# Kernel tuning notes

Measured on AMD Instinct MI355X. Metric: run time of the kernel, lower is better.

## Reference

```python
import jax, jax.numpy as jnp
import numpy as np

B, T, E = 8, 16384, 512
SEG = 16            # segment_count
DIL = 2             # dilation
DK = 64             # d_k
DV = 64             # d_v
POS_SCALE = 1.0     # pos_emb_scaling
L = T // SEG        # per-segment attention length before dilation (1024)
NORM = 1.0 / np.sqrt(DK)


def setup_inputs() -> dict:
    key = jax.random.key(0)
    k0, k1, k2, k3, k4 = jax.random.split(key, 5)
    x_in = jax.random.normal(k0, (B, T, E), dtype=jnp.float32)
    # parameters are drawn randn(k, m)/sqrt(k) in the original build
    Wk = jax.random.normal(k1, (DK, E), dtype=jnp.float32) / np.sqrt(DK)
    Wq = jax.random.normal(k2, (DK, E), dtype=jnp.float32) / np.sqrt(DK)
    Wv = jax.random.normal(k3, (DV, E), dtype=jnp.float32) / np.sqrt(DK)
    positional_embeddings_KQ = jax.random.normal(k4, (L, L), dtype=jnp.float32)
    return {"x_in": x_in, "Wk": Wk, "Wq": Wq, "Wv": Wv,
            "positional_embeddings_KQ": positional_embeddings_KQ}


def reference(x_in, Wk, Wq, Wv, positional_embeddings_KQ):
    # x_view: (B, SEG, E, L), then dilate last (time-within-segment) axis
    xv = x_in.reshape(B, L, SEG, E).transpose(0, 2, 3, 1)[:, :, :, ::DIL]  # (B,SEG,E,Ld)
    Q = jnp.einsum('bsel,ke->bslk', xv, Wq)  # (B,SEG,Ld,DK)
    K = jnp.einsum('bsel,ke->bslk', xv, Wk)
    V = jnp.einsum('bsel,ke->bslk', xv, Wv)  # (B,SEG,Ld,DV)
    # KQ[b,s,k,m] = <K_k, Q_m>
    KQ = jnp.einsum('bskd,bsmd->bskm', K, Q)  # (B,SEG,Ld,Ld)
    # causal tril mask, dilated; mask-fill with -inf (multiply-then-fill == where)
    mask = jnp.tril(jnp.ones((L, L), dtype=bool))[::DIL, ::DIL]
    KQ = jnp.where(mask, KQ, -jnp.inf)
    # positional bias (added after masking, as in the original)
    p = (positional_embeddings_KQ * POS_SCALE)[:L, :L][::DIL, ::DIL]
    KQ = KQ + p
    # NOTE: faithful to original — softmax over dim 3 (the Q/m axis)
    smKQ = jax.nn.softmax(KQ * NORM, axis=3)
    # att[b,s,m,d] = sum_n smKQ[b,s,n,m] * V[b,s,n,d]
    att = jnp.einsum('bsnm,bsnd->bsmd', smKQ, V)  # (B,SEG,Ld,DV)
    Ld = att.shape[2]
    # 'same' padding: strided scatter into zero-initialized (B,T,DV)
    res = jnp.zeros((B, T, DV), dtype=x_in.dtype)
    res = res.at[:, ::DIL, :].set(att.reshape(B, SEG * Ld, DV))
    return res
```

## Files before the change

### kernel.cpp

```cpp
#include <hip/hip_runtime.h>
#include <stdint.h>

typedef __attribute__((ext_vector_type(4))) float f32x4;
typedef __attribute__((ext_vector_type(8))) short bf16x8;
typedef __attribute__((ext_vector_type(4))) unsigned int u32x4;

#define C_NORM_LOG2E 0.18033688011112043f

__device__ __forceinline__ uint32_t swz(uint32_t a) { return a ^ (((a >> 7) & 7u) << 4); }
__device__ __forceinline__ uint32_t swzP(uint32_t a) { return a ^ (((a >> 7) & 3u) << 4); }

__device__ __forceinline__ uint32_t cvt_pk_bf16(float a, float b) {
  uint32_t r;
  asm("v_cvt_pk_bf16_f32 %0, %1, %2" : "=v"(r) : "v"(a), "v"(b));
  return r;
}

__device__ __forceinline__ float2 unpk_bf16(uint32_t u) {
  float2 f;
  f.x = __uint_as_float(u << 16);
  f.y = __uint_as_float(u & 0xffff0000u);
  return f;
}

__device__ __forceinline__ ushort f2bf(float f) {
  uint32_t u = __float_as_uint(f);
  u += 0x7FFFu + ((u >> 16) & 1u);
  return (ushort)(u >> 16);
}

__device__ __forceinline__ void gl_lds16(const void* gp, void* lp) {
  __builtin_amdgcn_global_load_lds((const __attribute__((address_space(1))) void*)gp,
                                   (__attribute__((address_space(3))) void*)lp, 16, 0, 0);
}

__global__ void pack_kernel(const float* __restrict__ Wk, const float* __restrict__ Wq,
                            const float* __restrict__ Wv, const float* __restrict__ PE,
                            ushort* __restrict__ Wp, float* __restrict__ PEdT) {
  int bid = blockIdx.x;
  if (bid < 384) {
    int i = bid * 256 + threadIdx.x;
    int n = i >> 9, e = i & 511;
    float val = (n < 64) ? Wq[n * 512 + e]
              : (n < 128) ? Wk[(n - 64) * 512 + e]
                          : Wv[(n - 128) * 512 + e];
    Wp[i] = f2bf(val);
  } else {
    int i = (bid - 384) * 256 + threadIdx.x;
    int m = i >> 9, n = i & 511;
    PEdT[i] = PE[n * 2048 + m * 2] * C_NORM_LOG2E;
  }
}

__global__ __launch_bounds__(512, 4) void proj_kernel(
    const float* __restrict__ x, const ushort* __restrict__ Wp,
    ushort* __restrict__ Qw, ushort* __restrict__ Kw, ushort* __restrict__ Vw) {
  __shared__ float Xl[2][8192];
  const int tid = threadIdx.x;
  const int lane = tid & 63, w = tid >> 6, g = lane >> 4, l15 = lane & 15;
  const int wr = w >> 2, wc = w & 3;
  const int bid = blockIdx.x;
  const int xcd = bid & 7, idx = bid >> 3;
  const int part = idx & 3, h = idx >> 2;
  const int bs = h * 8 + xcd;
  const int m0 = part * 128;
  const int R0 = bs * 512 + m0;
  const int b = bs >> 4, s = bs & 15;
  const char* xb = (const char*)x + ((size_t)b * 8388608 + (size_t)s * 512) * 4;

  f32x4 acc[4][3];
#pragma unroll
  for (int i = 0; i < 4; ++i)
#pragma unroll
    for (int j = 0; j < 3; ++j) acc[i][j] = (f32x4){0.f, 0.f, 0.f, 0.f};

  auto stage = [&](int kt, int buf) {
#pragma unroll
    for (int j = 0; j < 4; ++j) {
      uint32_t sl = (uint32_t)(j * 8192 + tid * 16);
      uint32_t t = sl ^ (((sl >> 8) & 7u) << 4);
      uint32_t row = t >> 8, colb = t & 255u;
      const char* src = xb + (size_t)(m0 + row) * 65536 + (size_t)kt * 256 + colb;
      gl_lds16(src, (char*)&Xl[buf][0] + sl);
    }
  };

  stage(0, 0);
  __syncthreads();
#pragma unroll
  for (int kt = 0; kt < 8; ++kt) {
    const int buf = kt & 1;
    if (kt < 7) stage(kt + 1, buf ^ 1);
#pragma unroll
    for (int kd = 0; kd < 2; ++kd) {
      bf16x8 bb[3];
#pragma unroll
      for (int j = 0; j < 3; ++j)
        bb[j] = *(const bf16x8*)((const char*)Wp + (size_t)(wc * 48 + j * 16 + l15) * 1024 +
                                 kt * 128 + kd * 64 + g * 16);
      bf16x8 a[4];
#pragma unroll
      for (int i = 0; i < 4; ++i) {
        int Rr = wr * 64 + i * 16 + l15;
        uint32_t a32 = (uint32_t)(Rr * 256 + kd * 128 + g * 32);
        uint32_t off0 = a32 ^ ((uint32_t)(Rr & 7) << 4);
        uint32_t off1 = off0 ^ 16u;
        f32x4 lo = *(const f32x4*)((const char*)&Xl[buf][0] + off0);
        f32x4 hi = *(const f32x4*)((const char*)&Xl[buf][0] + off1);
        uint32_t uu[4];
        uu[0] = cvt_pk_bf16(lo[0], lo[1]);
        uu[1] = cvt_pk_bf16(lo[2], lo[3]);
        uu[2] = cvt_pk_bf16(hi[0], hi[1]);
        uu[3] = cvt_pk_bf16(hi[2], hi[3]);
        a[i] = *(bf16x8*)uu;
      }
#pragma unroll
      for (int i = 0; i < 4; ++i)
#pragma unroll
        for (int j = 0; j < 3; ++j)
          acc[i][j] = __builtin_amdgcn_mfma_f32_16x16x32_bf16(a[i], bb[j], acc[i][j], 0, 0, 0);
    }
    __syncthreads();
  }
#pragma unroll
  for (int i = 0; i < 4; ++i) {
    int rl2 = wr * 64 + i * 16 + g * 4;
    size_t rbase = (size_t)(R0 + rl2) * 64;
#pragma unroll
    for (int j = 0; j < 3; ++j) {
      int n = wc * 48 + j * 16 + l15;
      int sel = n >> 6, d = n & 63;
      ushort* dst = (sel == 0) ? Qw : (sel == 1) ? Kw : Vw;
      dst += rbase + d;
#pragma unroll
      for (int r = 0; r < 4; ++r) dst[(size_t)r * 64] = f2bf(acc[i][j][r]);
    }
  }
}

__global__ __launch_bounds__(512, 4) void attn_kernel(
    const ushort* __restrict__ Qw, const ushort* __restrict__ Kw,
    const ushort* __restrict__ Vw, const float* __restrict__ PEdT,
    ushort* __restrict__ Pp) {
  __shared__ char Vtl[16384];
  __shared__ char Ptl[32768];
  __shared__ float red[512];
  __shared__ float rZrow[64];

  const int tid = threadIdx.x;
  const int w = tid >> 6, lane = tid & 63, g = lane >> 4, l15 = lane & 15;
  const int bid = blockIdx.x;
  const int xcd = bid & 7, idx = bid >> 3;
  const int bs = (idx & 15) * 8 + xcd;
  const int co = idx >> 4;
  const int c = co ^ (co >> 1);
  const int nmf = c + 1;
  const int wb = w * 16 * nmf;
  const size_t base = (size_t)bs * 32768;
  const char* Qb = (const char*)(Qw + base);
  const char* Kb = (const char*)(Kw + base);
  const char* Vb = (const char*)(Vw + base);
  char* Pw = Ptl + w * 4096;

  const int vrow = tid >> 3, vseg = tid & 7;
  auto scatter = [&](uint4 d4, int buf) {
    uint32_t dwv[4] = {d4.x, d4.y, d4.z, d4.w};
#pragma unroll
    for (int t = 0; t < 4; ++t) {
      int d0 = vseg * 8 + t * 2;
      *(ushort*)(Vtl + buf * 8192 + swz((uint32_t)(d0 * 128 + vrow * 2))) = (ushort)(dwv[t] & 0xffffu);
      *(ushort*)(Vtl + buf * 8192 + swz((uint32_t)((d0 + 1) * 128 + vrow * 2))) = (ushort)(dwv[t] >> 16);
    }
  };

  uint4 dv = *(const uint4*)(Vb + (size_t)(2 * c) * 8192 + vrow * 128 + vseg * 16);
  scatter(dv, 0);
  dv = *(const uint4*)(Vb + (size_t)(2 * c + 1) * 8192 + vrow * 128 + vseg * 16);
  __syncthreads();

  f32x4 att[4][4];
#pragma unroll
  for (int i = 0; i < 4; ++i)
#pragma unroll
    for (int j = 0; j < 4; ++j) att[i][j] = (f32x4){0.f, 0.f, 0.f, 0.f};

#pragma unroll
  for (int it = 0; it < 2; ++it) {
    const int nt = 2 * c + it;
    if (it == 0) scatter(dv, 1);

    uint32_t Ppk2[2][4][2];
    float ls[4][4];
#pragma unroll
    for (int nf = 0; nf < 4; ++nf) {
      bf16x8 aK[2];
#pragma unroll
      for (int kd = 0; kd < 2; ++kd)
        aK[kd] = *(const bf16x8*)(Kb + (size_t)nt * 8192 + (size_t)(nf * 16 + l15) * 128 +
                                  kd * 64 + g * 16);
      const int nb = nt * 64 + nf * 16 + g * 4;
      float l0 = 0.f, l1 = 0.f, l2 = 0.f, l3 = 0.f;
#pragma unroll
      for (int mf = 0; mf < 4; ++mf)
        if (mf < nmf) {
          const char* qrow = Qb + (size_t)(wb + mf * 16 + l15) * 128;
          bf16x8 q0 = *(const bf16x8*)(qrow + g * 16);
          bf16x8 q1 = *(const bf16x8*)(qrow + 64 + g * 16);
          f32x4 S = (f32x4){0.f, 0.f, 0.f, 0.f};
          S = __builtin_amdgcn_mfma_f32_16x16x32_bf16(aK[0], q0, S, 0, 0, 0);
          S = __builtin_amdgcn_mfma_f32_16x16x32_bf16(aK[1], q1, S, 0, 0, 0);
          int m_ = wb + mf * 16 + l15;
          f32x4 pe = *(const f32x4*)(PEdT + (size_t)m_ * 512 + nb);
          float e0 = (nb + 0 >= m_) ? exp2f(fmaf(S[0], C_NORM_LOG2E, pe[0])) : 0.f;
          float e1 = (nb + 1 >= m_) ? exp2f(fmaf(S[1], C_NORM_LOG2E, pe[1])) : 0.f;
          float e2 = (nb + 2 >= m_) ? exp2f(fmaf(S[2], C_NORM_LOG2E, pe[2])) : 0.f;
          float e3 = (nb + 3 >= m_) ? exp2f(fmaf(S[3], C_NORM_LOG2E, pe[3])) : 0.f;
          l0 += e0; l1 += e1; l2 += e2; l3 += e3;
          uint32_t ux = cvt_pk_bf16(e0, e1);
          uint32_t uy = cvt_pk_bf16(e2, e3);
          if (nf < 2) {
            uint2 u; u.x = ux; u.y = uy;
            *(uint2*)(Pw + swzP((uint32_t)((mf * 16 + l15) * 64 + (nf & 1) * 32 + g * 8))) = u;
          } else {
            Ppk2[nf - 2][mf][0] = ux;
            Ppk2[nf - 2][mf][1] = uy;
          }
        }
      ls[nf][0] = l0; ls[nf][1] = l1; ls[nf][2] = l2; ls[nf][3] = l3;
    }
#pragma unroll
    for (int msk = 1; msk < 16; msk <<= 1)
#pragma unroll
      for (int nf = 0; nf < 4; ++nf)
#pragma unroll
        for (int r = 0; r < 4; ++r) ls[nf][r] += __shfl_xor(ls[nf][r], msk, 16);
    if (l15 == 0) {
#pragma unroll
      for (int nf = 0; nf < 4; ++nf)
#pragma unroll
        for (int r = 0; r < 4; ++r) red[w * 64 + nf * 16 + g * 4 + r] = ls[nf][r];
    }
    __syncthreads();
    {
      int row8 = lane >> 3, srcw = lane & 7;
      float v = red[srcw * 64 + w * 8 + row8];
      v += __shfl_xor(v, 1);
      v += __shfl_xor(v, 2);
      v += __shfl_xor(v, 4);
      if (srcw == 0) rZrow[w * 8 + row8] = 1.0f / v;
    }
    __syncthreads();
#pragma unroll
    for (int kf = 0; kf < 2; ++kf) {
      if (kf == 1) {
#pragma unroll
        for (int nf2 = 0; nf2 < 2; ++nf2)
#pragma unroll
          for (int mf = 0; mf < 4; ++mf)
            if (mf < nmf) {
              uint2 u; u.x = Ppk2[nf2][mf][0]; u.y = Ppk2[nf2][mf][1];
              *(uint2*)(Pw + swzP((uint32_t)((mf * 16 + l15) * 64 + nf2 * 32 + g * 8))) = u;
            }
      }
      f32x4 za = *(const f32x4*)&rZrow[kf * 32 + g * 8];
      f32x4 zb = *(const f32x4*)&rZrow[kf * 32 + g * 8 + 4];
      bf16x8 bV[4];
#pragma unroll
      for (int df = 0; df < 4; ++df) {
        u32x4 vv = *(const u32x4*)(Vtl + it * 8192 +
                                   swz((uint32_t)((df * 16 + l15) * 128 + kf * 64 + g * 16)));
        uint32_t oo[4];
        float2 f0 = unpk_bf16(vv[0]);
        float2 f1 = unpk_bf16(vv[1]);
        float2 f2 = unpk_bf16(vv[2]);
        float2 f3 = unpk_bf16(vv[3]);
        oo[0] = cvt_pk_bf16(f0.x * za[0], f0.y * za[1]);
        oo[1] = cvt_pk_bf16(f1.x * za[2], f1.y * za[3]);
        oo[2] = cvt_pk_bf16(f2.x * zb[0], f2.y * zb[1]);
        oo[3] = cvt_pk_bf16(f3.x * zb[2], f3.y * zb[3]);
        bV[df] = *(bf16x8*)oo;
      }
#pragma unroll
      for (int mf = 0; mf < 4; ++mf)
        if (mf < nmf) {
          bf16x8 aP = *(const bf16x8*)(Pw + swzP((uint32_t)((mf * 16 + l15) * 64 + g * 16)));
#pragma unroll
          for (int df = 0; df < 4; ++df)
            att[mf][df] = __builtin_amdgcn_mfma_f32_16x16x32_bf16(aP, bV[df], att[mf][df], 0, 0, 0);
        }
    }
  }

  ushort* pb = Pp + ((size_t)c * 128 + bs) * 32768;
#pragma unroll
  for (int mf = 0; mf < 4; ++mf)
    if (mf < nmf) {
#pragma unroll
      for (int df = 0; df < 4; ++df)
#pragma unroll
        for (int r = 0; r < 4; ++r) {
          int m_ = wb + mf * 16 + g * 4 + r;
          pb[(size_t)m_ * 64 + df * 16 + l15] = f2bf(att[mf][df][r]);
        }
    }
}

__global__ void reduce_kernel(const ushort* __restrict__ Pp, float* __restrict__ out) {
  const int bid = blockIdx.x;
  const int xcd = bid & 7, idx = bid >> 3;
  const int bs = (idx & 15) * 8 + xcd;
  const int inner = idx >> 4;
  int jj = bs * 4096 + inner * 256 + threadIdx.x;
  int d8 = jj & 7, m = (jj >> 3) & 511;
  const size_t ji = ((size_t)bs * 512 + m) * 64 + d8 * 8;
  float f[8];
#pragma unroll
  for (int e = 0; e < 8; ++e) f[e] = 0.f;
  for (int cc = m >> 7; cc < 4; ++cc) {
    uint4 v = *(const uint4*)(Pp + (size_t)cc * 4194304 + ji);
    uint32_t dw[4] = {v.x, v.y, v.z, v.w};
#pragma unroll
    for (int t = 0; t < 4; ++t) {
      f[t * 2] += __uint_as_float(dw[t] << 16);
      f[t * 2 + 1] += __uint_as_float(dw[t] & 0xffff0000u);
    }
  }
  int b = bs >> 4, s = bs & 15;
  size_t t0 = 2 * ((size_t)s * 512 + m);
  float* ob = out + (size_t)b * 1048576 + t0 * 64 + d8 * 8;
  *(float4*)(ob) = (float4){f[0], f[1], f[2], f[3]};
  *(float4*)(ob + 4) = (float4){f[4], f[5], f[6], f[7]};
  *(float4*)(ob + 64) = (float4){0.f, 0.f, 0.f, 0.f};
  *(float4*)(ob + 68) = (float4){0.f, 0.f, 0.f, 0.f};
}

extern "C" void kernel_launch(void* const* d_in, const int* in_sizes, int n_in,
                              void* d_out, int out_size, void* d_ws, size_t ws_size,
                              hipStream_t stream) {
  const float* x  = (const float*)d_in[0];
  const float* Wk = (const float*)d_in[1];
  const float* Wq = (const float*)d_in[2];
  const float* Wv = (const float*)d_in[3];
  const float* PE = (const float*)d_in[4];
  float* out = (float*)d_out;
  char* ws = (char*)d_ws;

  ushort* Qw   = (ushort*)(ws);
  ushort* Kw   = (ushort*)(ws + 8388608);
  ushort* Vw   = (ushort*)(ws + 16777216);
  ushort* Wp   = (ushort*)(ws + 25165824);
  float*  PEdT = (float*)(ws + 25362432);
  ushort* Pp   = (ushort*)(ws + 33554432);

  pack_kernel<<<dim3(1408), dim3(256), 0, stream>>>(Wk, Wq, Wv, PE, Wp, PEdT);
  proj_kernel<<<dim3(512), dim3(512), 0, stream>>>(x, Wp, Qw, Kw, Vw);
  attn_kernel<<<dim3(512), dim3(512), 0, stream>>>(Qw, Kw, Vw, PEdT, Pp);
  reduce_kernel<<<dim3(2048), dim3(256), 0, stream>>>(Pp, out);
}
```

Baseline: 113.8 us.

## Fuse partial-sum reduction into attention kernel via last-block atomic counter

```diff
diff --git a/kernel.cpp b/kernel.cpp
--- a/kernel.cpp
+++ b/kernel.cpp
@@ -36,7 +36,8 @@
 
 __global__ void pack_kernel(const float* __restrict__ Wk, const float* __restrict__ Wq,
                             const float* __restrict__ Wv, const float* __restrict__ PE,
-                            ushort* __restrict__ Wp, float* __restrict__ PEdT) {
+                            ushort* __restrict__ Wp, float* __restrict__ PEdT,
+                            unsigned* __restrict__ cnt, float* __restrict__ out) {
   int bid = blockIdx.x;
   if (bid < 384) {
     int i = bid * 256 + threadIdx.x;
@@ -45,10 +46,21 @@
               : (n < 128) ? Wk[(n - 64) * 512 + e]
                           : Wv[(n - 128) * 512 + e];
     Wp[i] = f2bf(val);
-  } else {
+  } else if (bid < 1408) {
     int i = (bid - 384) * 256 + threadIdx.x;
     int m = i >> 9, n = i & 511;
     PEdT[i] = PE[n * 2048 + m * 2] * C_NORM_LOG2E;
+    if (bid == 384 && threadIdx.x < 128) cnt[threadIdx.x] = 0u;
+  } else {
+    int zbid = bid - 1408;
+#pragma unroll
+    for (int k = 0; k < 4; ++k) {
+      int z = zbid * 1024 + k * 256 + threadIdx.x;
+      int b = z >> 17, zl = z & 131071;
+      int row_o = zl >> 4, d4 = zl & 15;
+      float* p = out + (size_t)b * 1048576 + (size_t)(2 * row_o + 1) * 64 + d4 * 4;
+      *(float4*)p = (float4){0.f, 0.f, 0.f, 0.f};
+    }
   }
 }
 
@@ -141,11 +153,12 @@
 __global__ __launch_bounds__(512, 4) void attn_kernel(
     const ushort* __restrict__ Qw, const ushort* __restrict__ Kw,
     const ushort* __restrict__ Vw, const float* __restrict__ PEdT,
-    ushort* __restrict__ Pp) {
+    ushort* __restrict__ Pp, unsigned* __restrict__ cnt, float* __restrict__ out) {
   __shared__ char Vtl[16384];
   __shared__ char Ptl[32768];
   __shared__ float red[512];
   __shared__ float rZrow[64];
+  __shared__ unsigned lastFlag;
 
   const int tid = threadIdx.x;
   const int w = tid >> 6, lane = tid & 63, g = lane >> 4, l15 = lane & 15;
@@ -303,35 +316,36 @@
           pb[(size_t)m_ * 64 + df * 16 + l15] = f2bf(att[mf][df][r]);
         }
     }
-}
-
-__global__ void reduce_kernel(const ushort* __restrict__ Pp, float* __restrict__ out) {
-  const int bid = blockIdx.x;
-  const int xcd = bid & 7, idx = bid >> 3;
-  const int bs = (idx & 15) * 8 + xcd;
-  const int inner = idx >> 4;
-  int jj = bs * 4096 + inner * 256 + threadIdx.x;
-  int d8 = jj & 7, m = (jj >> 3) & 511;
-  const size_t ji = ((size_t)bs * 512 + m) * 64 + d8 * 8;
-  float f[8];
-#pragma unroll
-  for (int e = 0; e < 8; ++e) f[e] = 0.f;
-  for (int cc = m >> 7; cc < 4; ++cc) {
-    uint4 v = *(const uint4*)(Pp + (size_t)cc * 4194304 + ji);
-    uint32_t dw[4] = {v.x, v.y, v.z, v.w};
-#pragma unroll
-    for (int t = 0; t < 4; ++t) {
-      f[t * 2] += __uint_as_float(dw[t] << 16);
-      f[t * 2 + 1] += __uint_as_float(dw[t] & 0xffff0000u);
-    }
-  }
-  int b = bs >> 4, s = bs & 15;
-  size_t t0 = 2 * ((size_t)s * 512 + m);
-  float* ob = out + (size_t)b * 1048576 + t0 * 64 + d8 * 8;
-  *(float4*)(ob) = (float4){f[0], f[1], f[2], f[3]};
-  *(float4*)(ob + 4) = (float4){f[4], f[5], f[6], f[7]};
-  *(float4*)(ob + 64) = (float4){0.f, 0.f, 0.f, 0.f};
-  *(float4*)(ob + 68) = (float4){0.f, 0.f, 0.f, 0.f};
+
+  __threadfence();
+  __syncthreads();
+  if (tid == 0) lastFlag = (atomicAdd(&cnt[bs], 1u) == 3u) ? 1u : 0u;
+  __syncthreads();
+  if (lastFlag == 0u) return;
+  __threadfence();
+  const int b = bs >> 4, s = bs & 15;
+  float* obase = out + (size_t)b * 1048576 + (size_t)s * 65536;
+#pragma unroll
+  for (int k = 0; k < 8; ++k) {
+    int jj = k * 512 + tid;
+    int d8 = jj & 7, m = jj >> 3;
+    const size_t ji = ((size_t)bs * 512 + m) * 64 + d8 * 8;
+    float f[8];
+#pragma unroll
+    for (int e = 0; e < 8; ++e) f[e] = 0.f;
+    for (int cc = m >> 7; cc < 4; ++cc) {
+      uint4 v = *(const uint4*)(Pp + (size_t)cc * 4194304 + ji);
+      uint32_t dw[4] = {v.x, v.y, v.z, v.w};
+#pragma unroll
+      for (int t = 0; t < 4; ++t) {
+        f[t * 2] += __uint_as_float(dw[t] << 16);
+        f[t * 2 + 1] += __uint_as_float(dw[t] & 0xffff0000u);
+      }
+    }
+    float* ob = obase + (size_t)m * 128 + d8 * 8;
+    *(float4*)(ob) = (float4){f[0], f[1], f[2], f[3]};
+    *(float4*)(ob + 4) = (float4){f[4], f[5], f[6], f[7]};
+  }
 }
 
 extern "C" void kernel_launch(void* const* d_in, const int* in_sizes, int n_in,
@@ -351,9 +365,9 @@
   ushort* Wp   = (ushort*)(ws + 25165824);
   float*  PEdT = (float*)(ws + 25362432);
   ushort* Pp   = (ushort*)(ws + 33554432);
-
-  pack_kernel<<<dim3(1408), dim3(256), 0, stream>>>(Wk, Wq, Wv, PE, Wp, PEdT);
+  unsigned* cnt = (unsigned*)(ws + 67108864);
+
+  pack_kernel<<<dim3(2432), dim3(256), 0, stream>>>(Wk, Wq, Wv, PE, Wp, PEdT, cnt, out);
   proj_kernel<<<dim3(512), dim3(512), 0, stream>>>(x, Wp, Qw, Kw, Vw);
-  attn_kernel<<<dim3(512), dim3(512), 0, stream>>>(Qw, Kw, Vw, PEdT, Pp);
-  reduce_kernel<<<dim3(2048), dim3(256), 0, stream>>>(Pp, out);
-}
+  attn_kernel<<<dim3(512), dim3(512), 0, stream>>>(Qw, Kw, Vw, PEdT, Pp, cnt, out);
+}
```

New measurement: 281.0 us. 147% more time.

## Precompute softmax normalizers in a separate pass and parallelize attention over query rows

Applied to the files above, without the earlier changes.

```diff
diff --git a/kernel.cpp b/kernel.cpp
--- a/kernel.cpp
+++ b/kernel.cpp
@@ -3,24 +3,15 @@
 
 typedef __attribute__((ext_vector_type(4))) float f32x4;
 typedef __attribute__((ext_vector_type(8))) short bf16x8;
-typedef __attribute__((ext_vector_type(4))) unsigned int u32x4;
 
 #define C_NORM_LOG2E 0.18033688011112043f
 
 __device__ __forceinline__ uint32_t swz(uint32_t a) { return a ^ (((a >> 7) & 7u) << 4); }
-__device__ __forceinline__ uint32_t swzP(uint32_t a) { return a ^ (((a >> 7) & 3u) << 4); }
 
 __device__ __forceinline__ uint32_t cvt_pk_bf16(float a, float b) {
   uint32_t r;
   asm("v_cvt_pk_bf16_f32 %0, %1, %2" : "=v"(r) : "v"(a), "v"(b));
   return r;
-}
-
-__device__ __forceinline__ float2 unpk_bf16(uint32_t u) {
-  float2 f;
-  f.x = __uint_as_float(u << 16);
-  f.y = __uint_as_float(u & 0xffff0000u);
-  return f;
 }
 
 __device__ __forceinline__ ushort f2bf(float f) {
@@ -138,200 +129,190 @@
   }
 }
 
+__global__ __launch_bounds__(512, 4) void zrec_kernel(
+    const ushort* __restrict__ Qw, const ushort* __restrict__ Kw,
+    const float* __restrict__ PEdT, float* __restrict__ rZ,
+    float* __restrict__ out) {
+  __shared__ char Ql[2][8192];
+  const int tid = threadIdx.x;
+  const int w = tid >> 6, lane = tid & 63, g = lane >> 4, l15 = lane & 15;
+  const int bid = blockIdx.x;
+  const int hi = bid >> 8, lo = bid & 255;
+  const int half = lo >> 7, bs = lo & 127;
+  const int nc = (hi << 1) | (half ^ hi);
+  const int b = bs >> 4, s = bs & 15;
+
+  {
+    float* ob = out + (size_t)b * 1048576;
+#pragma unroll
+    for (int k = 0; k < 4; ++k) {
+      int jj = k * 512 + tid;
+      int rowl = jj >> 4, d4 = jj & 15;
+      int mrow = nc * 128 + rowl;
+      float* p = ob + (size_t)(2 * (s * 512 + mrow) + 1) * 64 + d4 * 4;
+      *(float4*)p = (float4){0.f, 0.f, 0.f, 0.f};
+    }
+  }
+
+  const char* Qb = (const char*)(Qw + (size_t)bs * 32768);
+  const char* Kb = (const char*)(Kw + (size_t)bs * 32768);
+  const int nw0 = nc * 128 + w * 16;
+  bf16x8 aK0, aK1;
+  {
+    const char* kr = Kb + (size_t)(nw0 + l15) * 128;
+    aK0 = *(const bf16x8*)(kr + g * 16);
+    aK1 = *(const bf16x8*)(kr + 64 + g * 16);
+  }
+  const int NT = 2 * (nc + 1);
+  auto stage = [&](int mt, int buf) {
+    uint32_t sl = (uint32_t)(tid * 16);
+    uint32_t t = sl ^ (((sl >> 7) & 7u) << 4);
+    uint32_t row = t >> 7, colb = t & 127u;
+    gl_lds16(Qb + (size_t)(mt * 64 + row) * 128 + colb, (char*)&Ql[buf][0] + sl);
+  };
+  stage(0, 0);
+  float z0 = 0.f, z1 = 0.f, z2 = 0.f, z3 = 0.f;
+  __syncthreads();
+  for (int mt = 0; mt < NT; ++mt) {
+    const int buf = mt & 1;
+    if (mt + 1 < NT) stage(mt + 1, buf ^ 1);
+    if (mt * 64 <= nw0 + 15) {
+#pragma unroll
+      for (int mf = 0; mf < 4; ++mf) {
+        int mq = mf * 16 + l15;
+        bf16x8 q0 = *(const bf16x8*)((char*)&Ql[buf][0] + swz((uint32_t)(mq * 128 + g * 16)));
+        bf16x8 q1 = *(const bf16x8*)((char*)&Ql[buf][0] + swz((uint32_t)(mq * 128 + 64 + g * 16)));
+        f32x4 S = (f32x4){0.f, 0.f, 0.f, 0.f};
+        S = __builtin_amdgcn_mfma_f32_16x16x32_bf16(aK0, q0, S, 0, 0, 0);
+        S = __builtin_amdgcn_mfma_f32_16x16x32_bf16(aK1, q1, S, 0, 0, 0);
+        int m_ = mt * 64 + mq;
+        f32x4 pe = *(const f32x4*)(PEdT + (size_t)m_ * 512 + nw0 + g * 4);
+        int nr = nw0 + g * 4;
+        if (nr + 0 >= m_) z0 += exp2f(fmaf(S[0], C_NORM_LOG2E, pe[0]));
+        if (nr + 1 >= m_) z1 += exp2f(fmaf(S[1], C_NORM_LOG2E, pe[1]));
+        if (nr + 2 >= m_) z2 += exp2f(fmaf(S[2], C_NORM_LOG2E, pe[2]));
+        if (nr + 3 >= m_) z3 += exp2f(fmaf(S[3], C_NORM_LOG2E, pe[3]));
+      }
+    }
+    __syncthreads();
+  }
+#pragma unroll
+  for (int msk = 1; msk < 16; msk <<= 1) {
+    z0 += __shfl_xor(z0, msk, 16);
+    z1 += __shfl_xor(z1, msk, 16);
+    z2 += __shfl_xor(z2, msk, 16);
+    z3 += __shfl_xor(z3, msk, 16);
+  }
+  if (l15 == 0) {
+    float* zp = rZ + (size_t)bs * 512 + nw0 + g * 4;
+    zp[0] = 1.0f / z0;
+    zp[1] = 1.0f / z1;
+    zp[2] = 1.0f / z2;
+    zp[3] = 1.0f / z3;
+  }
+}
+
 __global__ __launch_bounds__(512, 4) void attn_kernel(
     const ushort* __restrict__ Qw, const ushort* __restrict__ Kw,
     const ushort* __restrict__ Vw, const float* __restrict__ PEdT,
-    ushort* __restrict__ Pp) {
-  __shared__ char Vtl[16384];
-  __shared__ char Ptl[32768];
-  __shared__ float red[512];
-  __shared__ float rZrow[64];
+    const float* __restrict__ rZ, float* __restrict__ out) {
+  __shared__ char Vtl[2][8192];
+  __shared__ char Ptl[8][2048];
 
   const int tid = threadIdx.x;
   const int w = tid >> 6, lane = tid & 63, g = lane >> 4, l15 = lane & 15;
   const int bid = blockIdx.x;
-  const int xcd = bid & 7, idx = bid >> 3;
-  const int bs = (idx & 15) * 8 + xcd;
-  const int co = idx >> 4;
-  const int c = co ^ (co >> 1);
-  const int nmf = c + 1;
-  const int wb = w * 16 * nmf;
+  const int hi = bid >> 8, lo = bid & 255;
+  const int half = lo >> 7, bs = lo & 127;
+  const int ms = (hi << 1) | (half ^ hi);
+  const int m0w = ms * 128 + w * 16;
   const size_t base = (size_t)bs * 32768;
   const char* Qb = (const char*)(Qw + base);
   const char* Kb = (const char*)(Kw + base);
   const char* Vb = (const char*)(Vw + base);
-  char* Pw = Ptl + w * 4096;
-
+  char* Pw = &Ptl[w][0];
+
+  bf16x8 bQ0, bQ1;
+  {
+    const char* qr = Qb + (size_t)(m0w + l15) * 128;
+    bQ0 = *(const bf16x8*)(qr + g * 16);
+    bQ1 = *(const bf16x8*)(qr + 64 + g * 16);
+  }
+
+  f32x4 acc[4];
+#pragma unroll
+  for (int j = 0; j < 4; ++j) acc[j] = (f32x4){0.f, 0.f, 0.f, 0.f};
+
+  const int t0 = 2 * ms, NTT = 8 - t0;
   const int vrow = tid >> 3, vseg = tid & 7;
   auto scatter = [&](uint4 d4, int buf) {
     uint32_t dwv[4] = {d4.x, d4.y, d4.z, d4.w};
 #pragma unroll
     for (int t = 0; t < 4; ++t) {
       int d0 = vseg * 8 + t * 2;
-      *(ushort*)(Vtl + buf * 8192 + swz((uint32_t)(d0 * 128 + vrow * 2))) = (ushort)(dwv[t] & 0xffffu);
-      *(ushort*)(Vtl + buf * 8192 + swz((uint32_t)((d0 + 1) * 128 + vrow * 2))) = (ushort)(dwv[t] >> 16);
+      *(ushort*)(&Vtl[buf][0] + swz((uint32_t)(d0 * 128 + vrow * 2))) = (ushort)(dwv[t] & 0xffffu);
+      *(ushort*)(&Vtl[buf][0] + swz((uint32_t)((d0 + 1) * 128 + vrow * 2))) = (ushort)(dwv[t] >> 16);
     }
   };
 
-  uint4 dv = *(const uint4*)(Vb + (size_t)(2 * c) * 8192 + vrow * 128 + vseg * 16);
+  uint4 dv = *(const uint4*)(Vb + (size_t)t0 * 8192 + vrow * 128 + vseg * 16);
   scatter(dv, 0);
-  dv = *(const uint4*)(Vb + (size_t)(2 * c + 1) * 8192 + vrow * 128 + vseg * 16);
+  if (NTT > 1) dv = *(const uint4*)(Vb + (size_t)(t0 + 1) * 8192 + vrow * 128 + vseg * 16);
   __syncthreads();
 
-  f32x4 att[4][4];
-#pragma unroll
-  for (int i = 0; i < 4; ++i)
-#pragma unroll
-    for (int j = 0; j < 4; ++j) att[i][j] = (f32x4){0.f, 0.f, 0.f, 0.f};
-
-#pragma unroll
-  for (int it = 0; it < 2; ++it) {
-    const int nt = 2 * c + it;
-    if (it == 0) scatter(dv, 1);
-
-    uint32_t Ppk2[2][4][2];
-    float ls[4][4];
-#pragma unroll
-    for (int nf = 0; nf < 4; ++nf) {
-      bf16x8 aK[2];
-#pragma unroll
-      for (int kd = 0; kd < 2; ++kd)
-        aK[kd] = *(const bf16x8*)(Kb + (size_t)nt * 8192 + (size_t)(nf * 16 + l15) * 128 +
-                                  kd * 64 + g * 16);
-      const int nb = nt * 64 + nf * 16 + g * 4;
-      float l0 = 0.f, l1 = 0.f, l2 = 0.f, l3 = 0.f;
-#pragma unroll
-      for (int mf = 0; mf < 4; ++mf)
-        if (mf < nmf) {
-          const char* qrow = Qb + (size_t)(wb + mf * 16 + l15) * 128;
-          bf16x8 q0 = *(const bf16x8*)(qrow + g * 16);
-          bf16x8 q1 = *(const bf16x8*)(qrow + 64 + g * 16);
-          f32x4 S = (f32x4){0.f, 0.f, 0.f, 0.f};
-          S = __builtin_amdgcn_mfma_f32_16x16x32_bf16(aK[0], q0, S, 0, 0, 0);
-          S = __builtin_amdgcn_mfma_f32_16x16x32_bf16(aK[1], q1, S, 0, 0, 0);
-          int m_ = wb + mf * 16 + l15;
-          f32x4 pe = *(const f32x4*)(PEdT + (size_t)m_ * 512 + nb);
-          float e0 = (nb + 0 >= m_) ? exp2f(fmaf(S[0], C_NORM_LOG2E, pe[0])) : 0.f;
-          float e1 = (nb + 1 >= m_) ? exp2f(fmaf(S[1], C_NORM_LOG2E, pe[1])) : 0.f;
-          float e2 = (nb + 2 >= m_) ? exp2f(fmaf(S[2], C_NORM_LOG2E, pe[2])) : 0.f;
-          float e3 = (nb + 3 >= m_) ? exp2f(fmaf(S[3], C_NORM_LOG2E, pe[3])) : 0.f;
-          l0 += e0; l1 += e1; l2 += e2; l3 += e3;
-          uint32_t ux = cvt_pk_bf16(e0, e1);
-          uint32_t uy = cvt_pk_bf16(e2, e3);
-          if (nf < 2) {
-            uint2 u; u.x = ux; u.y = uy;
-            *(uint2*)(Pw + swzP((uint32_t)((mf * 16 + l15) * 64 + (nf & 1) * 32 + g * 8))) = u;
-          } else {
-            Ppk2[nf - 2][mf][0] = ux;
-            Ppk2[nf - 2][mf][1] = uy;
-          }
+  for (int tt = 0; tt < NTT; ++tt) {
+    const int t = t0 + tt, buf = tt & 1;
+    if (tt + 1 < NTT) {
+      scatter(dv, buf ^ 1);
+      if (tt + 2 < NTT)
+        dv = *(const uint4*)(Vb + (size_t)(t + 2) * 8192 + vrow * 128 + vseg * 16);
+    }
+    const bool wact = (m0w <= t * 64 + 63);
+    if (wact) {
+      const int m_ = m0w + l15;
+#pragma unroll
+      for (int nf = 0; nf < 4; ++nf) {
+        const char* kr = Kb + (size_t)t * 8192 + (size_t)(nf * 16 + l15) * 128;
+        bf16x8 k0 = *(const bf16x8*)(kr + g * 16);
+        bf16x8 k1 = *(const bf16x8*)(kr + 64 + g * 16);
+        f32x4 S = (f32x4){0.f, 0.f, 0.f, 0.f};
+        S = __builtin_amdgcn_mfma_f32_16x16x32_bf16(k0, bQ0, S, 0, 0, 0);
+        S = __builtin_amdgcn_mfma_f32_16x16x32_bf16(k1, bQ1, S, 0, 0, 0);
+        const int nb = t * 64 + nf * 16 + g * 4;
+        f32x4 pe = *(const f32x4*)(PEdT + (size_t)m_ * 512 + nb);
+        f32x4 rz4 = *(const f32x4*)(rZ + (size_t)bs * 512 + nb);
+        float e0 = (nb + 0 >= m_) ? exp2f(fmaf(S[0], C_NORM_LOG2E, pe[0])) * rz4[0] : 0.f;
+        float e1 = (nb + 1 >= m_) ? exp2f(fmaf(S[1], C_NORM_LOG2E, pe[1])) * rz4[1] : 0.f;
+        float e2 = (nb + 2 >= m_) ? exp2f(fmaf(S[2], C_NORM_LOG2E, pe[2])) * rz4[2] : 0.f;
+        float e3 = (nb + 3 >= m_) ? exp2f(fmaf(S[3], C_NORM_LOG2E, pe[3])) * rz4[3] : 0.f;
+        uint2 u;
+        u.x = cvt_pk_bf16(e0, e1);
+        u.y = cvt_pk_bf16(e2, e3);
+        *(uint2*)(Pw + swz((uint32_t)(l15 * 128 + nf * 32 + g * 8))) = u;
+      }
+#pragma unroll
+      for (int kf = 0; kf < 2; ++kf) {
+        bf16x8 aP = *(const bf16x8*)(Pw + swz((uint32_t)(l15 * 128 + kf * 64 + g * 16)));
+#pragma unroll
+        for (int df = 0; df < 4; ++df) {
+          bf16x8 bV = *(const bf16x8*)(&Vtl[buf][0] +
+                                       swz((uint32_t)((df * 16 + l15) * 128 + kf * 64 + g * 16)));
+          acc[df] = __builtin_amdgcn_mfma_f32_16x16x32_bf16(aP, bV, acc[df], 0, 0, 0);
         }
-      ls[nf][0] = l0; ls[nf][1] = l1; ls[nf][2] = l2; ls[nf][3] = l3;
-    }
-#pragma unroll
-    for (int msk = 1; msk < 16; msk <<= 1)
-#pragma unroll
-      for (int nf = 0; nf < 4; ++nf)
-#pragma unroll
-        for (int r = 0; r < 4; ++r) ls[nf][r] += __shfl_xor(ls[nf][r], msk, 16);
-    if (l15 == 0) {
-#pragma unroll
-      for (int nf = 0; nf < 4; ++nf)
-#pragma unroll
-        for (int r = 0; r < 4; ++r) red[w * 64 + nf * 16 + g * 4 + r] = ls[nf][r];
+      }
     }
     __syncthreads();
-    {
-      int row8 = lane >> 3, srcw = lane & 7;
-      float v = red[srcw * 64 + w * 8 + row8];
-      v += __shfl_xor(v, 1);
-      v += __shfl_xor(v, 2);
-      v += __shfl_xor(v, 4);
-      if (srcw == 0) rZrow[w * 8 + row8] = 1.0f / v;
-    }
-    __syncthreads();
-#pragma unroll
-    for (int kf = 0; kf < 2; ++kf) {
-      if (kf == 1) {
-#pragma unroll
-        for (int nf2 = 0; nf2 < 2; ++nf2)
-#pragma unroll
-          for (int mf = 0; mf < 4; ++mf)
-            if (mf < nmf) {
-              uint2 u; u.x = Ppk2[nf2][mf][0]; u.y = Ppk2[nf2][mf][1];
-              *(uint2*)(Pw + swzP((uint32_t)((mf * 16 + l15) * 64 + nf2 * 32 + g * 8))) = u;
-            }
-      }
-      f32x4 za = *(const f32x4*)&rZrow[kf * 32 + g * 8];
-      f32x4 zb = *(const f32x4*)&rZrow[kf * 32 + g * 8 + 4];
-      bf16x8 bV[4];
-#pragma unroll
-      for (int df = 0; df < 4; ++df) {
-        u32x4 vv = *(const u32x4*)(Vtl + it * 8192 +
-                                   swz((uint32_t)((df * 16 + l15) * 128 + kf * 64 + g * 16)));
-        uint32_t oo[4];
-        float2 f0 = unpk_bf16(vv[0]);
-        float2 f1 = unpk_bf16(vv[1]);
-        float2 f2 = unpk_bf16(vv[2]);
-        float2 f3 = unpk_bf16(vv[3]);
-        oo[0] = cvt_pk_bf16(f0.x * za[0], f0.y * za[1]);
-        oo[1] = cvt_pk_bf16(f1.x * za[2], f1.y * za[3]);
-        oo[2] = cvt_pk_bf16(f2.x * zb[0], f2.y * zb[1]);
-        oo[3] = cvt_pk_bf16(f3.x * zb[2], f3.y * zb[3]);
-        bV[df] = *(bf16x8*)oo;
-      }
-#pragma unroll
-      for (int mf = 0; mf < 4; ++mf)
-        if (mf < nmf) {
-          bf16x8 aP = *(const bf16x8*)(Pw + swzP((uint32_t)((mf * 16 + l15) * 64 + g * 16)));
-#pragma unroll
-          for (int df = 0; df < 4; ++df)
-            att[mf][df] = __builtin_amdgcn_mfma_f32_16x16x32_bf16(aP, bV[df], att[mf][df], 0, 0, 0);
-        }
-    }
-  }
-
-  ushort* pb = Pp + ((size_t)c * 128 + bs) * 32768;
-#pragma unroll
-  for (int mf = 0; mf < 4; ++mf)
-    if (mf < nmf) {
-#pragma unroll
-      for (int df = 0; df < 4; ++df)
-#pragma unroll
-        for (int r = 0; r < 4; ++r) {
-          int m_ = wb + mf * 16 + g * 4 + r;
-          pb[(size_t)m_ * 64 + df * 16 + l15] = f2bf(att[mf][df][r]);
-        }
-    }
-}
-
-__global__ void reduce_kernel(const ushort* __restrict__ Pp, float* __restrict__ out) {
-  const int bid = blockIdx.x;
-  const int xcd = bid & 7, idx = bid >> 3;
-  const int bs = (idx & 15) * 8 + xcd;
-  const int inner = idx >> 4;
-  int jj = bs * 4096 + inner * 256 + threadIdx.x;
-  int d8 = jj & 7, m = (jj >> 3) & 511;
-  const size_t ji = ((size_t)bs * 512 + m) * 64 + d8 * 8;
-  float f[8];
-#pragma unroll
-  for (int e = 0; e < 8; ++e) f[e] = 0.f;
-  for (int cc = m >> 7; cc < 4; ++cc) {
-    uint4 v = *(const uint4*)(Pp + (size_t)cc * 4194304 + ji);
-    uint32_t dw[4] = {v.x, v.y, v.z, v.w};
-#pragma unroll
-    for (int t = 0; t < 4; ++t) {
-      f[t * 2] += __uint_as_float(dw[t] << 16);
-      f[t * 2 + 1] += __uint_as_float(dw[t] & 0xffff0000u);
-    }
-  }
-  int b = bs >> 4, s = bs & 15;
-  size_t t0 = 2 * ((size_t)s * 512 + m);
-  float* ob = out + (size_t)b * 1048576 + t0 * 64 + d8 * 8;
-  *(float4*)(ob) = (float4){f[0], f[1], f[2], f[3]};
-  *(float4*)(ob + 4) = (float4){f[4], f[5], f[6], f[7]};
-  *(float4*)(ob + 64) = (float4){0.f, 0.f, 0.f, 0.f};
-  *(float4*)(ob + 68) = (float4){0.f, 0.f, 0.f, 0.f};
+  }
+
+  const int b = bs >> 4, s = bs & 15;
+  float* ob = out + (size_t)b * 1048576;
+#pragma unroll
+  for (int df = 0; df < 4; ++df)
+#pragma unroll
+    for (int r = 0; r < 4; ++r) {
+      int m_ = m0w + g * 4 + r;
+      ob[(size_t)(2 * (s * 512 + m_)) * 64 + df * 16 + l15] = acc[df][r];
+    }
 }
 
 extern "C" void kernel_launch(void* const* d_in, const int* in_sizes, int n_in,
@@ -350,10 +331,10 @@
   ushort* Vw   = (ushort*)(ws + 16777216);
   ushort* Wp   = (ushort*)(ws + 25165824);
   float*  PEdT = (float*)(ws + 25362432);
-  ushort* Pp   = (ushort*)(ws + 33554432);
+  float*  rZ   = (float*)(ws + 26411008);
 
   pack_kernel<<<dim3(1408), dim3(256), 0, stream>>>(Wk, Wq, Wv, PE, Wp, PEdT);
   proj_kernel<<<dim3(512), dim3(512), 0, stream>>>(x, Wp, Qw, Kw, Vw);
-  attn_kernel<<<dim3(512), dim3(512), 0, stream>>>(Qw, Kw, Vw, PEdT, Pp);
-  reduce_kernel<<<dim3(2048), dim3(256), 0, stream>>>(Pp, out);
-}
+  zrec_kernel<<<dim3(512), dim3(512), 0, stream>>>(Qw, Kw, PEdT, rZ, out);
+  attn_kernel<<<dim3(512), dim3(512), 0, stream>>>(Qw, Kw, Vw, PEdT, rZ, out);
+}
```

Measured after the change: 101.1 us. 11.2% less time.
